# Kernel optimization log

Hardware: AMD Instinct MI355X
Metric: run time of the kernel (lower is better)

The kernel has to match this reference:

```python
import jax, jax.numpy as jnp
import numpy as np

D_MODEL = 1024
NUM_HEADS = 16
D_HEAD = D_MODEL // NUM_HEADS
THETA = 10000.0
NEG_INF = -1e9


def apply_rope(x, theta=THETA):
    # x: (..., S, Dh) with interleaved pairs (2i, 2i+1)
    S, Dh = x.shape[-2], x.shape[-1]
    inv_freq = 1.0 / (theta ** (jnp.arange(0, Dh, 2, dtype=jnp.float32) / Dh))  # (Dh/2,)
    ang = jnp.arange(S, dtype=jnp.float32)[:, None] * inv_freq[None, :]          # (S, Dh/2)
    cos, sin = jnp.cos(ang), jnp.sin(ang)
    x1 = x[..., 0::2]
    x2 = x[..., 1::2]
    r1 = x1 * cos - x2 * sin
    r2 = x1 * sin + x2 * cos
    # interleave back
    return jnp.stack([r1, r2], axis=-1).reshape(x.shape)


def setup_inputs() -> dict:
    key = jax.random.key(0)
    ks = jax.random.split(key, 5)
    B, S = 2, 2048
    scale = 1.0 / np.sqrt(D_MODEL)
    return {
        "x": jax.random.normal(ks[0], (B, S, D_MODEL), dtype=jnp.float32),
        "Wq": jax.random.normal(ks[1], (D_MODEL, D_MODEL), dtype=jnp.float32) * scale,
        "Wk": jax.random.normal(ks[2], (D_MODEL, D_MODEL), dtype=jnp.float32) * scale,
        "Wv": jax.random.normal(ks[3], (D_MODEL, D_MODEL), dtype=jnp.float32) * scale,
        "Wo": jax.random.normal(ks[4], (D_MODEL, D_MODEL), dtype=jnp.float32) * scale,
    }


def reference(x, Wq, Wk, Wv, Wo):
    B, S, _ = x.shape
    def split_heads(t):
        return t.reshape(B, S, NUM_HEADS, D_HEAD).transpose(0, 2, 1, 3)  # (B,H,S,Dh)
    # nn.Linear(bias=False): y = x @ W.T
    Q = split_heads(x @ Wq.T)
    K = split_heads(x @ Wk.T)
    V = split_heads(x @ Wv.T)
    Q = apply_rope(Q)
    K = apply_rope(K)
    scale = 1.0 / jnp.sqrt(jnp.asarray(D_HEAD, dtype=x.dtype))
    scores = jnp.einsum("bhqd,bhkd->bhqk", Q, K) * scale  # (B,H,S,S)
    causal = jnp.tril(jnp.ones((S, S), dtype=bool))
    scores = jnp.where(causal, scores, NEG_INF)
    attn = jax.nn.softmax(scores, axis=-1)
    out = jnp.einsum("bhqk,bhkd->bhqd", attn, V)
    out = out.transpose(0, 2, 1, 3).reshape(B, S, D_MODEL)
    return out @ Wo.T
```

## Files before the change

kernel.cpp:

```cpp
#include <hip/hip_runtime.h>
#include <hip/hip_bf16.h>
#include <stdint.h>

typedef __attribute__((ext_vector_type(8))) short bf8;
typedef __attribute__((ext_vector_type(4))) float f4;

#define MFMA16(a, b, c) __builtin_amdgcn_mfma_f32_16x16x32_bf16((a), (b), (c), 0, 0, 0)

static __device__ __forceinline__ short f2b(float f) {
  uint32_t x = __float_as_uint(f);
  x += 0x7fffu + ((x >> 16) & 1u);
  return (short)(x >> 16);
}

static __device__ __forceinline__ uint32_t pk2(float a, float b) {
  return ((__float_as_uint(a) + 0x8000u) >> 16) |
         ((__float_as_uint(b) + 0x8000u) & 0xffff0000u);
}

static __device__ __forceinline__ void gload16(const short* g, void* l) {
  __builtin_amdgcn_global_load_lds(
      (const __attribute__((address_space(1))) void*)g,
      (__attribute__((address_space(3))) void*)l, 16, 0, 0);
}

__global__ void rope_kernel(float2* __restrict__ tab) {
  const int t = blockIdx.x * 256 + threadIdx.x;
  const int s = t >> 5, i = t & 31;
  const float inv = powf(10000.0f, -(float)i * (1.0f / 32.0f));
  const float ang = (float)s * inv;
  float sv, cv;
  sincosf(ang, &sv, &cv);
  tab[t] = make_float2(cv, sv);
}

__global__ void convert_kernel(const float* __restrict__ x,
                               const float* __restrict__ wq, const float* __restrict__ wk,
                               const float* __restrict__ wv, const float* __restrict__ wo,
                               short* __restrict__ xb, short* __restrict__ Wb) {
  const size_t i = ((size_t)blockIdx.x * 256 + threadIdx.x) * 8;
  const float* __restrict__ src;
  short* __restrict__ dst;
  if (i < 4194304u) {
    src = x + i;
    dst = xb + i;
  } else {
    const size_t j = i - 4194304u;
    const int z = (int)(j >> 20);
    const size_t o = j & 1048575u;
    src = (z == 0 ? wq : z == 1 ? wk : z == 2 ? wv : wo) + o;
    dst = Wb + j;
  }
  const float4 a = *(const float4*)src;
  const float4 b = *(const float4*)(src + 4);
  bf8 v;
  v[0] = f2b(a.x); v[1] = f2b(a.y); v[2] = f2b(a.z); v[3] = f2b(a.w);
  v[4] = f2b(b.x); v[5] = f2b(b.y); v[6] = f2b(b.z); v[7] = f2b(b.w);
  *(bf8*)dst = v;
}

template <int MODE>
__launch_bounds__(256, 2)
__global__ void gemm_kernel(const short* __restrict__ Ab, const short* __restrict__ Wb,
                            short* __restrict__ Qo, short* __restrict__ Ko,
                            short* __restrict__ VTo, float* __restrict__ Fo,
                            const float2* __restrict__ rope) {
  constexpr int K = 1024;
  const int bm = blockIdx.x, bn = blockIdx.y;
  const int z = (MODE == 0) ? blockIdx.z : 3;
  const short* __restrict__ Bb = Wb + ((size_t)z << 20);

  __shared__ short As[128 * 64];
  __shared__ short Bs[128 * 64];

  const int tid = threadIdx.x;
  const int lane = tid & 63;
  const int wave = tid >> 6;
  const int wr = wave >> 1, wc = wave & 1;
  const int lg = lane >> 4, lr = lane & 15;

  f4 acc[4][4];
#pragma unroll
  for (int i = 0; i < 4; i++)
#pragma unroll
    for (int j = 0; j < 4; j++) {
      acc[i][j][0] = 0.f; acc[i][j][1] = 0.f;
      acc[i][j][2] = 0.f; acc[i][j][3] = 0.f;
    }

  const int kc = tid & 7;
  const int srow = tid >> 3;
  const int kcs = (kc ^ (srow & 7)) * 8;
  char* const Asw = (char*)As + wave * 1024;
  char* const Bsw = (char*)Bs + wave * 1024;

  for (int k0 = 0; k0 < K; k0 += 64) {
#pragma unroll
    for (int i = 0; i < 4; i++) {
      const int row = srow + i * 32;
      gload16(Ab + (size_t)(bm * 128 + row) * K + k0 + kcs, Asw + i * 4096);
      gload16(Bb + (size_t)(bn * 128 + row) * K + k0 + kcs, Bsw + i * 4096);
    }
    __syncthreads();
#pragma unroll
    for (int kk = 0; kk < 2; kk++) {
      bf8 af[4], bb[4];
#pragma unroll
      for (int mi = 0; mi < 4; mi++) {
        const int row = wr * 64 + mi * 16 + lr;
        const int lb = (row * 128 + kk * 64 + lg * 16) ^ ((row & 7) << 4);
        af[mi] = *(const bf8*)((const char*)As + lb);
      }
#pragma unroll
      for (int ni = 0; ni < 4; ni++) {
        const int row = wc * 64 + ni * 16 + lr;
        const int lb = (row * 128 + kk * 64 + lg * 16) ^ ((row & 7) << 4);
        bb[ni] = *(const bf8*)((const char*)Bs + lb);
      }
#pragma unroll
      for (int mi = 0; mi < 4; mi++)
#pragma unroll
        for (int ni = 0; ni < 4; ni++)
          acc[mi][ni] = MFMA16(af[mi], bb[ni], acc[mi][ni]);
    }
    __syncthreads();
  }

  if (MODE == 1) {
#pragma unroll
    for (int mi = 0; mi < 4; mi++) {
      const int m0 = bm * 128 + wr * 64 + mi * 16 + lg * 4;
#pragma unroll
      for (int ni = 0; ni < 4; ni++) {
        const int n = bn * 128 + wc * 64 + ni * 16 + lr;
#pragma unroll
        for (int r = 0; r < 4; r++)
          Fo[(size_t)(m0 + r) * 1024 + n] = acc[mi][ni][r];
      }
    }
    return;
  }

  if (z == 2) {
#pragma unroll
    for (int mi = 0; mi < 4; mi++) {
      const int m0 = bm * 128 + wr * 64 + mi * 16 + lg * 4;
      const int b = m0 >> 11, s0 = m0 & 2047;
#pragma unroll
      for (int ni = 0; ni < 4; ni++) {
        const int n = bn * 128 + wc * 64 + ni * 16 + lr;
        ushort4 pk;
        pk.x = (unsigned short)f2b(acc[mi][ni][0]);
        pk.y = (unsigned short)f2b(acc[mi][ni][1]);
        pk.z = (unsigned short)f2b(acc[mi][ni][2]);
        pk.w = (unsigned short)f2b(acc[mi][ni][3]);
        *(ushort4*)(VTo + ((size_t)((b * 16 + (n >> 6)) * 64 + (n & 63))) * 2048 + s0) = pk;
      }
    }
  } else {
    short* __restrict__ Out = (z == 0) ? Qo : Ko;
    const float qscale = (z == 0) ? 0.18033688011112042f : 1.0f;
#pragma unroll
    for (int mi = 0; mi < 4; mi++) {
      const int m0 = bm * 128 + wr * 64 + mi * 16 + lg * 4;
      const int b = m0 >> 11, s0 = m0 & 2047;
#pragma unroll
      for (int ni = 0; ni < 4; ni++) {
        const int n = bn * 128 + wc * 64 + ni * 16 + lr;
        const int h = n >> 6, d = n & 63;
        const float sgn = (d & 1) ? 1.0f : -1.0f;
#pragma unroll
        for (int r = 0; r < 4; r++) {
          const float v = acc[mi][ni][r];
          const float p = __shfl_xor(v, 1);
          const float2 cs = rope[((s0 + r) << 5) + (d >> 1)];
          const float res = (v * cs.x + sgn * p * cs.y) * qscale;
          Out[((size_t)(b * 16 + h) * 2048 + (s0 + r)) * 64 + d] = f2b(res);
        }
      }
    }
  }
}

__launch_bounds__(512, 4)
__global__ void attn_kernel(const short* __restrict__ Qg, const short* __restrict__ Kg,
                            const short* __restrict__ Vg, short* __restrict__ AO) {
  const int S = 2048;
  const int id = blockIdx.x;
  const int xcd = id & 7, slot = id >> 3;
  const int bh = xcd * 4 + (slot & 3);
  const int qb = 15 - (slot >> 2);
  const int tid = threadIdx.x;
  const int lane = tid & 63, wave = tid >> 6;
  const int lg = lane >> 4, lr = lane & 15;
  const short* __restrict__ Qp = Qg + (size_t)bh * S * 64;
  const short* __restrict__ Kp = Kg + (size_t)bh * S * 64;
  const short* __restrict__ Vp = Vg + (size_t)bh * 64 * S;

  __shared__ short KB[2][64 * 64];
  __shared__ short VB[2][64 * 64];
  __shared__ short PB[8][16 * 64];

  const int srow = tid >> 3;
  const int kcs = ((tid & 7) ^ (srow & 7)) * 8;
  const size_t ksrc = (size_t)srow * 64 + kcs;
  const size_t vsrc = (size_t)srow * 2048 + kcs;

  const int qbase = qb * 128 + wave * 16;
  const int my_nkv = (qbase + 79) >> 6;
  const int blk_nkv = (qb * 128 + 191) >> 6;

  bf8 qf[2];
#pragma unroll
  for (int ks = 0; ks < 2; ks++)
    qf[ks] = *(const bf8*)(Qp + (size_t)(qbase + lr) * 64 + ks * 32 + lg * 8);

  f4 o[4];
#pragma unroll
  for (int dt = 0; dt < 4; dt++) {
    o[dt][0] = 0.f; o[dt][1] = 0.f; o[dt][2] = 0.f; o[dt][3] = 0.f;
  }
  float mrun = -1e30f, lsum = 0.f;

  char* const Pw = (char*)&PB[wave][0];
  const int rowoff = lr * 128;
  const int sw = (lr & 7) << 4;

  gload16(Kp + ksrc, (char*)KB[0] + wave * 1024);
  gload16(Vp + vsrc, (char*)VB[0] + wave * 1024);
  __syncthreads();

  for (int kb = 0; kb < blk_nkv; kb++) {
    const int kvb = kb * 64;
    const int cur = kb & 1;

    if (kb + 1 < blk_nkv) {
      gload16(Kp + (size_t)(kvb + 64) * 64 + ksrc, (char*)KB[cur ^ 1] + wave * 1024);
      gload16(Vp + (size_t)(kvb + 64) + vsrc, (char*)VB[cur ^ 1] + wave * 1024);
    }

    if (kb < my_nkv) {
      const char* Kc = (const char*)KB[cur];
      const char* Vc = (const char*)VB[cur];

      f4 st[4];
      __builtin_amdgcn_s_setprio(1);
#pragma unroll
      for (int nt = 0; nt < 4; nt++) {
        const int row = nt * 16 + lr;
        const int base = row * 128 + lg * 16;
        const int rsw = (row & 7) << 4;
        const bf8 k0 = *(const bf8*)(Kc + ((base) ^ rsw));
        const bf8 k1 = *(const bf8*)(Kc + ((base + 64) ^ rsw));
        f4 c;
        c[0] = 0.f; c[1] = 0.f; c[2] = 0.f; c[3] = 0.f;
        c = MFMA16(k0, qf[0], c);
        c = MFMA16(k1, qf[1], c);
        st[nt] = c;
      }
      __builtin_amdgcn_s_setprio(0);

      if ((kvb + 63) > qbase) {
        const int q = qbase + lr;
#pragma unroll
        for (int nt = 0; nt < 4; nt++)
#pragma unroll
          for (int r = 0; r < 4; r++) {
            const int kv = kvb + nt * 16 + lg * 4 + r;
            if (kv > q) st[nt][r] = -1e9f;
          }
      }

      float m0 = fmaxf(fmaxf(st[0][0], st[0][1]), fmaxf(st[0][2], st[0][3]));
#pragma unroll
      for (int nt = 1; nt < 4; nt++)
        m0 = fmaxf(m0, fmaxf(fmaxf(st[nt][0], st[nt][1]), fmaxf(st[nt][2], st[nt][3])));
      m0 = fmaxf(m0, __shfl_xor(m0, 16));
      m0 = fmaxf(m0, __shfl_xor(m0, 32));

      if (__any(m0 - mrun > 8.0f)) {
        const float mn = fmaxf(mrun, m0);
        const float corr = __builtin_amdgcn_exp2f(mrun - mn);
        mrun = mn;
        lsum *= corr;
#pragma unroll
        for (int r = 0; r < 4; r++) {
          const float co = __shfl(corr, (lg << 2) + r);
#pragma unroll
          for (int dt = 0; dt < 4; dt++) o[dt][r] *= co;
        }
      }

      asm volatile("s_waitcnt lgkmcnt(0)" ::: "memory");

#pragma unroll
      for (int nt = 0; nt < 4; nt++) {
        const float p0 = __builtin_amdgcn_exp2f(st[nt][0] - mrun);
        const float p1 = __builtin_amdgcn_exp2f(st[nt][1] - mrun);
        const float p2 = __builtin_amdgcn_exp2f(st[nt][2] - mrun);
        const float p3 = __builtin_amdgcn_exp2f(st[nt][3] - mrun);
        lsum += (p0 + p1) + (p2 + p3);
        *(uint2*)(Pw + ((rowoff + nt * 32 + lg * 8) ^ sw)) = make_uint2(pk2(p0, p1), pk2(p2, p3));
      }

      asm volatile("s_waitcnt lgkmcnt(0)" ::: "memory");

      bf8 pf[2];
#pragma unroll
      for (int ks = 0; ks < 2; ks++)
        pf[ks] = *(const bf8*)(Pw + ((rowoff + ks * 64 + lg * 16) ^ sw));

      __builtin_amdgcn_s_setprio(1);
#pragma unroll
      for (int dt = 0; dt < 4; dt++) {
        const int row = dt * 16 + lr;
        const int base = row * 128 + lg * 16;
        const int rsw = (row & 7) << 4;
        const bf8 v0 = *(const bf8*)(Vc + ((base) ^ rsw));
        const bf8 v1 = *(const bf8*)(Vc + ((base + 64) ^ rsw));
        o[dt] = MFMA16(pf[0], v0, o[dt]);
        o[dt] = MFMA16(pf[1], v1, o[dt]);
      }
      __builtin_amdgcn_s_setprio(0);
    }

    __syncthreads();
  }

  float s = lsum;
  s += __shfl_xor(s, 16);
  s += __shfl_xor(s, 32);
  const float inv = 1.0f / s;
  float inv_o[4];
#pragma unroll
  for (int r = 0; r < 4; r++) inv_o[r] = __shfl(inv, (lg << 2) + r);

  const int b = bh >> 4, h = bh & 15;
#pragma unroll
  for (int r = 0; r < 4; r++) {
    const int q = qbase + lg * 4 + r;
#pragma unroll
    for (int dt = 0; dt < 4; dt++) {
      const int d = dt * 16 + lr;
      AO[((size_t)b * 2048 + q) * 1024 + h * 64 + d] = f2b(o[dt][r] * inv_o[r]);
    }
  }
}

extern "C" void kernel_launch(void* const* d_in, const int* in_sizes, int n_in,
                              void* d_out, int out_size, void* d_ws, size_t ws_size,
                              hipStream_t stream) {
  const float* x  = (const float*)d_in[0];
  const float* wq = (const float*)d_in[1];
  const float* wk = (const float*)d_in[2];
  const float* wv = (const float*)d_in[3];
  const float* wo = (const float*)d_in[4];
  float* out = (float*)d_out;

  char* ws = (char*)d_ws;
  short*  Qb  = (short*)(ws);
  short*  Kb  = (short*)(ws + (8ull  << 20));
  short*  VTb = (short*)(ws + (16ull << 20));
  short*  AOb = (short*)(ws + (24ull << 20));
  short*  xb  = AOb;
  short*  Wb  = (short*)(ws + (32ull << 20));
  float2* tab = (float2*)(ws + (40ull << 20));

  convert_kernel<<<4096, 256, 0, stream>>>(x, wq, wk, wv, wo, xb, Wb);
  rope_kernel<<<256, 256, 0, stream>>>(tab);
  gemm_kernel<0><<<dim3(32, 8, 3), 256, 0, stream>>>(
      xb, Wb, Qb, Kb, VTb, nullptr, tab);
  attn_kernel<<<512, 512, 0, stream>>>(Qb, Kb, VTb, AOb);
  gemm_kernel<1><<<dim3(32, 8, 1), 256, 0, stream>>>(
      AOb, Wb, nullptr, nullptr, nullptr, out, nullptr);
}
```

Baseline: 114.7 us.

## Pair causal query tiles per wave for balanced attention work and K/V fragment reuse

Measured after the change: 117.3 us. +2.3%, slower.

```diff
diff --git a/kernel.cpp b/kernel.cpp
--- a/kernel.cpp
+++ b/kernel.cpp
@@ -182,14 +182,14 @@
   }
 }
 
-__launch_bounds__(512, 4)
+__launch_bounds__(256, 2)
 __global__ void attn_kernel(const short* __restrict__ Qg, const short* __restrict__ Kg,
                             const short* __restrict__ Vg, short* __restrict__ AO) {
   const int S = 2048;
   const int id = blockIdx.x;
-  const int xcd = id & 7, slot = id >> 3;
-  const int bh = xcd * 4 + (slot & 3);
-  const int qb = 15 - (slot >> 2);
+  const int xcd = id & 7, r = id >> 3;
+  const int bh = xcd * 4 + (r & 3);
+  const int i = r >> 2;
   const int tid = threadIdx.x;
   const int lane = tid & 63, wave = tid >> 6;
   const int lg = lane >> 4, lr = lane & 15;
@@ -199,152 +199,187 @@
 
   __shared__ short KB[2][64 * 64];
   __shared__ short VB[2][64 * 64];
-  __shared__ short PB[8][16 * 64];
-
-  const int srow = tid >> 3;
-  const int kcs = ((tid & 7) ^ (srow & 7)) * 8;
-  const size_t ksrc = (size_t)srow * 64 + kcs;
-  const size_t vsrc = (size_t)srow * 2048 + kcs;
-
-  const int qbase = qb * 128 + wave * 16;
-  const int my_nkv = (qbase + 79) >> 6;
-  const int blk_nkv = (qb * 128 + 191) >> 6;
-
-  bf8 qf[2];
-#pragma unroll
-  for (int ks = 0; ks < 2; ks++)
-    qf[ks] = *(const bf8*)(Qp + (size_t)(qbase + lr) * 64 + ks * 32 + lg * 8);
-
-  f4 o[4];
-#pragma unroll
-  for (int dt = 0; dt < 4; dt++) {
-    o[dt][0] = 0.f; o[dt][1] = 0.f; o[dt][2] = 0.f; o[dt][3] = 0.f;
-  }
-  float mrun = -1e30f, lsum = 0.f;
-
-  char* const Pw = (char*)&PB[wave][0];
+  __shared__ short PB[4][2][16 * 64];
+
+  const int tL = 16 * wave + i;
+  const int tH = 127 - tL;
+  const int qbaseT[2] = {tH << 4, tL << 4};
+  const int nkvT[2] = {(16 * tH + 79) >> 6, (16 * tL + 79) >> 6};
+  const int blk_nkv = (2111 - 16 * i) >> 6;
+
+  const int rsub = lane >> 3;
+  const int chsw = ((lane & 7) ^ rsub) * 8;
+  const int row0 = (2 * wave) * 8 + rsub;
+  const int row1 = (2 * wave + 1) * 8 + rsub;
+  char* const kd0 = (char*)nullptr;
+
+#define STAGE_KV(buf, kvb_)                                                        \
+  do {                                                                             \
+    gload16(Kp + (size_t)((kvb_) + row0) * 64 + chsw, (char*)KB[buf] + (2 * wave) * 1024);     \
+    gload16(Kp + (size_t)((kvb_) + row1) * 64 + chsw, (char*)KB[buf] + (2 * wave + 1) * 1024); \
+    gload16(Vp + (size_t)row0 * 2048 + (kvb_) + chsw, (char*)VB[buf] + (2 * wave) * 1024);     \
+    gload16(Vp + (size_t)row1 * 2048 + (kvb_) + chsw, (char*)VB[buf] + (2 * wave + 1) * 1024); \
+  } while (0)
+
+  bf8 qf[2][2];
+#pragma unroll
+  for (int tt = 0; tt < 2; tt++)
+#pragma unroll
+    for (int ks = 0; ks < 2; ks++)
+      qf[tt][ks] = *(const bf8*)(Qp + (size_t)(qbaseT[tt] + lr) * 64 + ks * 32 + lg * 8);
+
+  f4 o[2][4];
+#pragma unroll
+  for (int tt = 0; tt < 2; tt++)
+#pragma unroll
+    for (int dt = 0; dt < 4; dt++) {
+      o[tt][dt][0] = 0.f; o[tt][dt][1] = 0.f; o[tt][dt][2] = 0.f; o[tt][dt][3] = 0.f;
+    }
+  float mrun[2] = {-1e30f, -1e30f};
+  float lsum[2] = {0.f, 0.f};
+
+  char* const PwT[2] = {(char*)&PB[wave][0][0], (char*)&PB[wave][1][0]};
   const int rowoff = lr * 128;
   const int sw = (lr & 7) << 4;
 
-  gload16(Kp + ksrc, (char*)KB[0] + wave * 1024);
-  gload16(Vp + vsrc, (char*)VB[0] + wave * 1024);
+  STAGE_KV(0, 0);
   __syncthreads();
 
   for (int kb = 0; kb < blk_nkv; kb++) {
     const int kvb = kb * 64;
     const int cur = kb & 1;
 
-    if (kb + 1 < blk_nkv) {
-      gload16(Kp + (size_t)(kvb + 64) * 64 + ksrc, (char*)KB[cur ^ 1] + wave * 1024);
-      gload16(Vp + (size_t)(kvb + 64) + vsrc, (char*)VB[cur ^ 1] + wave * 1024);
-    }
-
-    if (kb < my_nkv) {
+    if (kb + 1 < blk_nkv) STAGE_KV(cur ^ 1, kvb + 64);
+
+    if (kb < nkvT[0]) {
       const char* Kc = (const char*)KB[cur];
       const char* Vc = (const char*)VB[cur];
 
-      f4 st[4];
-      __builtin_amdgcn_s_setprio(1);
+      bf8 kf[4][2];
 #pragma unroll
       for (int nt = 0; nt < 4; nt++) {
         const int row = nt * 16 + lr;
         const int base = row * 128 + lg * 16;
         const int rsw = (row & 7) << 4;
-        const bf8 k0 = *(const bf8*)(Kc + ((base) ^ rsw));
-        const bf8 k1 = *(const bf8*)(Kc + ((base + 64) ^ rsw));
-        f4 c;
-        c[0] = 0.f; c[1] = 0.f; c[2] = 0.f; c[3] = 0.f;
-        c = MFMA16(k0, qf[0], c);
-        c = MFMA16(k1, qf[1], c);
-        st[nt] = c;
-      }
-      __builtin_amdgcn_s_setprio(0);
-
-      if ((kvb + 63) > qbase) {
-        const int q = qbase + lr;
-#pragma unroll
-        for (int nt = 0; nt < 4; nt++)
-#pragma unroll
-          for (int r = 0; r < 4; r++) {
-            const int kv = kvb + nt * 16 + lg * 4 + r;
-            if (kv > q) st[nt][r] = -1e9f;
+        kf[nt][0] = *(const bf8*)(Kc + (base ^ rsw));
+        kf[nt][1] = *(const bf8*)(Kc + ((base + 64) ^ rsw));
+      }
+
+      asm volatile("s_waitcnt lgkmcnt(0)" ::: "memory");
+
+#pragma unroll
+      for (int tt = 0; tt < 2; tt++) {
+        if (kb < nkvT[tt]) {
+          f4 st[4];
+          __builtin_amdgcn_s_setprio(1);
+#pragma unroll
+          for (int nt = 0; nt < 4; nt++) {
+            f4 c;
+            c[0] = 0.f; c[1] = 0.f; c[2] = 0.f; c[3] = 0.f;
+            c = MFMA16(kf[nt][0], qf[tt][0], c);
+            c = MFMA16(kf[nt][1], qf[tt][1], c);
+            st[nt] = c;
           }
-      }
-
-      float m0 = fmaxf(fmaxf(st[0][0], st[0][1]), fmaxf(st[0][2], st[0][3]));
-#pragma unroll
-      for (int nt = 1; nt < 4; nt++)
-        m0 = fmaxf(m0, fmaxf(fmaxf(st[nt][0], st[nt][1]), fmaxf(st[nt][2], st[nt][3])));
-      m0 = fmaxf(m0, __shfl_xor(m0, 16));
-      m0 = fmaxf(m0, __shfl_xor(m0, 32));
-
-      if (__any(m0 - mrun > 8.0f)) {
-        const float mn = fmaxf(mrun, m0);
-        const float corr = __builtin_amdgcn_exp2f(mrun - mn);
-        mrun = mn;
-        lsum *= corr;
-#pragma unroll
-        for (int r = 0; r < 4; r++) {
-          const float co = __shfl(corr, (lg << 2) + r);
-#pragma unroll
-          for (int dt = 0; dt < 4; dt++) o[dt][r] *= co;
+          __builtin_amdgcn_s_setprio(0);
+
+          if ((kvb + 63) > qbaseT[tt]) {
+            const int q = qbaseT[tt] + lr;
+#pragma unroll
+            for (int nt = 0; nt < 4; nt++)
+#pragma unroll
+              for (int rr = 0; rr < 4; rr++) {
+                const int kv = kvb + nt * 16 + lg * 4 + rr;
+                if (kv > q) st[nt][rr] = -1e9f;
+              }
+          }
+
+          float m0 = fmaxf(fmaxf(st[0][0], st[0][1]), fmaxf(st[0][2], st[0][3]));
+#pragma unroll
+          for (int nt = 1; nt < 4; nt++)
+            m0 = fmaxf(m0, fmaxf(fmaxf(st[nt][0], st[nt][1]), fmaxf(st[nt][2], st[nt][3])));
+          m0 = fmaxf(m0, __shfl_xor(m0, 16));
+          m0 = fmaxf(m0, __shfl_xor(m0, 32));
+
+          if (__any(m0 - mrun[tt] > 8.0f)) {
+            const float mn = fmaxf(mrun[tt], m0);
+            const float corr = __builtin_amdgcn_exp2f(mrun[tt] - mn);
+            mrun[tt] = mn;
+            lsum[tt] *= corr;
+#pragma unroll
+            for (int rr = 0; rr < 4; rr++) {
+              const float co = __shfl(corr, (lg << 2) + rr);
+#pragma unroll
+              for (int dt = 0; dt < 4; dt++) o[tt][dt][rr] *= co;
+            }
+          }
+
+#pragma unroll
+          for (int nt = 0; nt < 4; nt++) {
+            const float p0 = __builtin_amdgcn_exp2f(st[nt][0] - mrun[tt]);
+            const float p1 = __builtin_amdgcn_exp2f(st[nt][1] - mrun[tt]);
+            const float p2 = __builtin_amdgcn_exp2f(st[nt][2] - mrun[tt]);
+            const float p3 = __builtin_amdgcn_exp2f(st[nt][3] - mrun[tt]);
+            lsum[tt] += (p0 + p1) + (p2 + p3);
+            *(uint2*)(PwT[tt] + ((rowoff + nt * 32 + lg * 8) ^ sw)) =
+                make_uint2(pk2(p0, p1), pk2(p2, p3));
+          }
         }
       }
 
       asm volatile("s_waitcnt lgkmcnt(0)" ::: "memory");
 
-#pragma unroll
-      for (int nt = 0; nt < 4; nt++) {
-        const float p0 = __builtin_amdgcn_exp2f(st[nt][0] - mrun);
-        const float p1 = __builtin_amdgcn_exp2f(st[nt][1] - mrun);
-        const float p2 = __builtin_amdgcn_exp2f(st[nt][2] - mrun);
-        const float p3 = __builtin_amdgcn_exp2f(st[nt][3] - mrun);
-        lsum += (p0 + p1) + (p2 + p3);
-        *(uint2*)(Pw + ((rowoff + nt * 32 + lg * 8) ^ sw)) = make_uint2(pk2(p0, p1), pk2(p2, p3));
-      }
-
-      asm volatile("s_waitcnt lgkmcnt(0)" ::: "memory");
-
-      bf8 pf[2];
-#pragma unroll
-      for (int ks = 0; ks < 2; ks++)
-        pf[ks] = *(const bf8*)(Pw + ((rowoff + ks * 64 + lg * 16) ^ sw));
-
-      __builtin_amdgcn_s_setprio(1);
+      bf8 vf[4][2];
 #pragma unroll
       for (int dt = 0; dt < 4; dt++) {
         const int row = dt * 16 + lr;
         const int base = row * 128 + lg * 16;
         const int rsw = (row & 7) << 4;
-        const bf8 v0 = *(const bf8*)(Vc + ((base) ^ rsw));
-        const bf8 v1 = *(const bf8*)(Vc + ((base + 64) ^ rsw));
-        o[dt] = MFMA16(pf[0], v0, o[dt]);
-        o[dt] = MFMA16(pf[1], v1, o[dt]);
-      }
-      __builtin_amdgcn_s_setprio(0);
+        vf[dt][0] = *(const bf8*)(Vc + (base ^ rsw));
+        vf[dt][1] = *(const bf8*)(Vc + ((base + 64) ^ rsw));
+      }
+
+#pragma unroll
+      for (int tt = 0; tt < 2; tt++) {
+        if (kb < nkvT[tt]) {
+          bf8 pf[2];
+#pragma unroll
+          for (int ks = 0; ks < 2; ks++)
+            pf[ks] = *(const bf8*)(PwT[tt] + ((rowoff + ks * 64 + lg * 16) ^ sw));
+          __builtin_amdgcn_s_setprio(1);
+#pragma unroll
+          for (int dt = 0; dt < 4; dt++) {
+            o[tt][dt] = MFMA16(pf[0], vf[dt][0], o[tt][dt]);
+            o[tt][dt] = MFMA16(pf[1], vf[dt][1], o[tt][dt]);
+          }
+          __builtin_amdgcn_s_setprio(0);
+        }
+      }
     }
 
     __syncthreads();
   }
 
-  float s = lsum;
-  s += __shfl_xor(s, 16);
-  s += __shfl_xor(s, 32);
-  const float inv = 1.0f / s;
-  float inv_o[4];
-#pragma unroll
-  for (int r = 0; r < 4; r++) inv_o[r] = __shfl(inv, (lg << 2) + r);
-
   const int b = bh >> 4, h = bh & 15;
 #pragma unroll
-  for (int r = 0; r < 4; r++) {
-    const int q = qbase + lg * 4 + r;
-#pragma unroll
-    for (int dt = 0; dt < 4; dt++) {
-      const int d = dt * 16 + lr;
-      AO[((size_t)b * 2048 + q) * 1024 + h * 64 + d] = f2b(o[dt][r] * inv_o[r]);
-    }
-  }
+  for (int tt = 0; tt < 2; tt++) {
+    float s = lsum[tt];
+    s += __shfl_xor(s, 16);
+    s += __shfl_xor(s, 32);
+    const float inv = 1.0f / s;
+    float inv_o[4];
+#pragma unroll
+    for (int rr = 0; rr < 4; rr++) inv_o[rr] = __shfl(inv, (lg << 2) + rr);
+#pragma unroll
+    for (int rr = 0; rr < 4; rr++) {
+      const int q = qbaseT[tt] + lg * 4 + rr;
+#pragma unroll
+      for (int dt = 0; dt < 4; dt++) {
+        const int d = dt * 16 + lr;
+        AO[((size_t)b * 2048 + q) * 1024 + h * 64 + d] = f2b(o[tt][dt][rr] * inv_o[rr]);
+      }
+    }
+  }
+#undef STAGE_KV
 }
 
 extern "C" void kernel_launch(void* const* d_in, const int* in_sizes, int n_in,
@@ -370,7 +405,7 @@
   rope_kernel<<<256, 256, 0, stream>>>(tab);
   gemm_kernel<0><<<dim3(32, 8, 3), 256, 0, stream>>>(
       xb, Wb, Qb, Kb, VTb, nullptr, tab);
-  attn_kernel<<<512, 512, 0, stream>>>(Qb, Kb, VTb, AOb);
+  attn_kernel<<<512, 256, 0, stream>>>(Qb, Kb, VTb, AOb);
   gemm_kernel<1><<<dim3(32, 8, 1), 256, 0, stream>>>(
       AOb, Wb, nullptr, nullptr, nullptr, out, nullptr);
 }
```
